# Performance work log

Hardware: AMD Instinct MI355X
Metric: run time of the kernel (lower is better)

The kernel has to match this reference:

```python
import jax, jax.numpy as jnp
import numpy as np
import math

EPS = 1e-5  # torch LayerNorm default


def entmax15(z):
    # Peters & Martins exact sort-based alpha=1.5 entmax along last axis.
    z = z / 2.0
    z = z - jnp.max(z, axis=-1, keepdims=True)
    zs = -jnp.sort(-z, axis=-1)                      # descending
    K = z.shape[-1]
    rho = jnp.arange(1, K + 1, dtype=z.dtype)
    mean = jnp.cumsum(zs, axis=-1) / rho
    mean_sq = jnp.cumsum(zs * zs, axis=-1) / rho
    ss = rho * (mean_sq - mean * mean)
    delta = jnp.clip((1.0 - ss) / rho, 0.0)
    tau = mean - jnp.sqrt(delta)
    k = jnp.sum(tau <= zs, axis=-1, keepdims=True)   # support size
    tau_star = jnp.take_along_axis(tau, k - 1, axis=-1)
    p = jnp.square(jnp.clip(z - tau_star, 0.0))
    return p


def mish(x):
    return x * jnp.tanh(jax.nn.softplus(x))


def layer_norm(x, g, b):
    mu = jnp.mean(x, axis=-1, keepdims=True)
    var = jnp.var(x, axis=-1, keepdims=True)
    return (x - mu) / jnp.sqrt(var + EPS) * g + b


def setup_inputs() -> dict:
    key = jax.random.key(0)
    D, H, F = 512, 8, 2048
    B, S = 8, 1024
    ks = jax.random.split(key, 16)
    s = 1.0 / math.sqrt(D)
    inp = {
        "x": jax.random.normal(ks[0], (B, S, D), jnp.float32),
        # weights stored [in, out]; y = x @ W + b
        "Wq": jax.random.normal(ks[1], (D, D), jnp.float32) * s,
        "bq": jnp.zeros((D,), jnp.float32),
        "Wk": jax.random.normal(ks[2], (D, D), jnp.float32) * s,
        "bk": jnp.zeros((D,), jnp.float32),
        "Wv": jax.random.normal(ks[3], (D, D), jnp.float32) * s,
        "bv": jnp.zeros((D,), jnp.float32),
        "Wo": jax.random.normal(ks[4], (D, D), jnp.float32) * s,
        "bo": jnp.zeros((D,), jnp.float32),
        "g1": jnp.ones((D,), jnp.float32),
        "be1": jnp.zeros((D,), jnp.float32),
        "W1": jax.random.normal(ks[5], (D, F), jnp.float32) * s,
        "b1": jnp.zeros((F,), jnp.float32),
        "W2": jax.random.normal(ks[6], (F, D), jnp.float32) * (1.0 / math.sqrt(F)),
        "b2": jnp.zeros((D,), jnp.float32),
        "g2": jnp.ones((D,), jnp.float32),
        "be2": jnp.zeros((D,), jnp.float32),
    }
    return inp


def reference(x, Wq, bq, Wk, bk, Wv, bv, Wo, bo, g1, be1, W1, b1, W2, b2, g2, be2):
    B, S, D = x.shape
    H = 8
    hd = D // H
    # multi-head self-attention (z = x)
    q = (x @ Wq + bq).reshape(B, S, H, hd).transpose(0, 2, 1, 3)
    k = (x @ Wk + bk).reshape(B, S, H, hd).transpose(0, 2, 1, 3)
    v = (x @ Wv + bv).reshape(B, S, H, hd).transpose(0, 2, 1, 3)
    scores = jnp.einsum("bhqd,bhkd->bhqk", q, k) / math.sqrt(hd)
    attn = entmax15(scores)
    out = jnp.einsum("bhqk,bhkd->bhqd", attn, v)
    out = out.transpose(0, 2, 1, 3).reshape(B, S, D)
    y = out @ Wo + bo
    x = x + layer_norm(y, g1, be1)
    # feed-forward with Mish
    y = mish(x @ W1 + b1) @ W2 + b2
    x = x + layer_norm(y, g2, be2)
    return x
```

## Files before the change

### kernel.cpp

```cpp
#include <hip/hip_runtime.h>


typedef float f32x4 __attribute__((ext_vector_type(4)));
typedef __bf16 b8 __attribute__((ext_vector_type(8)));

#define DEV static __device__ __forceinline__

DEV unsigned short f2bf(float f) {
  unsigned u = __float_as_uint(f);
  u += 0x7fffu + ((u >> 16) & 1u);
  return (unsigned short)(u >> 16);
}
DEV float bf2f(unsigned short b) { return __uint_as_float(((unsigned)b) << 16); }

DEV float mishf(float x) {
  if (x > 20.f) return x;
  float e = __expf(x);
  float u = 1.f + e;
  u *= u;
  return x * ((u - 1.f) / (u + 1.f));
}

DEV void async16(const void* g, void* l) {
  __builtin_amdgcn_global_load_lds(
      (const __attribute__((address_space(1))) unsigned int*)g,
      (__attribute__((address_space(3))) unsigned int*)l, 16, 0, 0);
}

template <int WM, int WN, int EPI, bool OUTBF>
__global__ __launch_bounds__(256) void gemm_bt(
    const unsigned short* __restrict__ A, const unsigned short* __restrict__ Bt,
    const float* __restrict__ bias, void* __restrict__ Cp,
    int K, int lda, int ldb, int ldc,
    long sA1, long sA2, long sB1, long sB2, long sC1, long sC2,
    int hdiv, float alpha) {
  constexpr int BM = WM * 64, BN = WN * 64;
  __shared__ unsigned short smA[BM * 32];
  __shared__ unsigned short smB[BN * 32];

  const int tid = threadIdx.x;
  const int lane = tid & 63;
  const int z = blockIdx.z;
  const long zi = z / hdiv, zr = z % hdiv;
  const unsigned short* Ab = A + zi * sA1 + zr * sA2 + (long)blockIdx.x * BM * lda;
  const unsigned short* Bb = Bt + zi * sB1 + zr * sB2 + (long)blockIdx.y * BN * ldb;

  int siA[WM];
  const unsigned short* gA[WM];
#pragma unroll
  for (int q = 0; q < WM; ++q) {
    int si = q * 256 + tid;
    int m = si >> 2, s = si & 3, g = s ^ ((m >> 1) & 3);
    siA[q] = si;
    gA[q] = Ab + (long)m * lda + g * 8;
  }
  int siB[WN];
  const unsigned short* gB[WN];
#pragma unroll
  for (int q = 0; q < WN; ++q) {
    int si = q * 256 + tid;
    int m = si >> 2, s = si & 3, g = s ^ ((m >> 1) & 3);
    siB[q] = si;
    gB[q] = Bb + (long)m * ldb + g * 8;
  }

  const int w = tid >> 6;
  const int wr = w / WN, wc = w % WN;
  const int fm = lane & 15, fg = lane >> 4;

  int aOff[4], bOff[4];
#pragma unroll
  for (int i = 0; i < 4; ++i) {
    int m = wr * 64 + i * 16 + fm;
    aOff[i] = (m * 4 + (fg ^ ((m >> 1) & 3))) * 8;
    int n = wc * 64 + i * 16 + fm;
    bOff[i] = (n * 4 + (fg ^ ((n >> 1) & 3))) * 8;
  }

  f32x4 acc[4][4];
#pragma unroll
  for (int i = 0; i < 4; ++i)
#pragma unroll
    for (int j = 0; j < 4; ++j) acc[i][j] = (f32x4){0.f, 0.f, 0.f, 0.f};

  for (int k0 = 0; k0 < K; k0 += 32) {
    __syncthreads();
#pragma unroll
    for (int q = 0; q < WM; ++q) async16(gA[q] + k0, (void*)&smA[siA[q] * 8]);
#pragma unroll
    for (int q = 0; q < WN; ++q) async16(gB[q] + k0, (void*)&smB[siB[q] * 8]);
    __syncthreads();

    b8 aF[4], bF[4];
#pragma unroll
    for (int i = 0; i < 4; ++i) aF[i] = *(const b8*)&smA[aOff[i]];
#pragma unroll
    for (int j = 0; j < 4; ++j) bF[j] = *(const b8*)&smB[bOff[j]];
#pragma unroll
    for (int i = 0; i < 4; ++i)
#pragma unroll
      for (int j = 0; j < 4; ++j)
        acc[i][j] = __builtin_amdgcn_mfma_f32_16x16x32_bf16(aF[i], bF[j], acc[i][j], 0, 0, 0);
  }

  const long cbase = zi * sC1 + zr * sC2;
  const int row0 = blockIdx.x * BM + wr * 64 + fg * 4;
  const int col0 = blockIdx.y * BN + wc * 64 + fm;
#pragma unroll
  for (int i = 0; i < 4; ++i) {
#pragma unroll
    for (int j = 0; j < 4; ++j) {
      const int col = col0 + j * 16;
      float bv = (EPI >= 1) ? bias[col] : 0.f;
#pragma unroll
      for (int r = 0; r < 4; ++r) {
        const int row = row0 + i * 16 + r;
        float v = acc[i][j][r] * alpha + bv;
        if (EPI == 2) v = mishf(v);
        const long idx = cbase + (long)row * ldc + col;
        if constexpr (OUTBF)
          ((unsigned short*)Cp)[idx] = f2bf(v);
        else
          ((float*)Cp)[idx] = v;
      }
    }
  }
}

__global__ __launch_bounds__(256) void entmax_rows(unsigned short* __restrict__ P) {
  const int tid = threadIdx.x, lane = tid & 63, wv = tid >> 6;
  const long row = (long)blockIdx.x * 4 + wv;
  unsigned short* p = P + row * 1024;

  union { uint4 v; unsigned short u[8]; } a, b;
  a.v = *(const uint4*)(p + lane * 16);
  b.v = *(const uint4*)(p + lane * 16 + 8);
  float zv[16];
#pragma unroll
  for (int i = 0; i < 8; ++i) {
    zv[i] = bf2f(a.u[i]);
    zv[8 + i] = bf2f(b.u[i]);
  }

  float m = zv[0];
#pragma unroll
  for (int i = 1; i < 16; ++i) m = fmaxf(m, zv[i]);
#pragma unroll
  for (int o = 32; o; o >>= 1) m = fmaxf(m, __shfl_xor(m, o));
#pragma unroll
  for (int i = 0; i < 16; ++i) zv[i] -= m;

  float tau = -1.f;
  int kprev = -1;
  for (int it = 0; it < 12; ++it) {
    float s1 = 0.f, s2 = 0.f;
    int k = 0;
#pragma unroll
    for (int i = 0; i < 16; ++i) {
      float h = zv[i] - tau;
      k += __popcll(__ballot(h > 0.f));
      float hp = fmaxf(h, 0.f);
      s1 += hp;
      s2 = fmaf(hp, hp, s2);
    }
#pragma unroll
    for (int o = 32; o; o >>= 1) {
      s1 += __shfl_xor(s1, o);
      s2 += __shfl_xor(s2, o);
    }
    if (k == kprev) break;
    kprev = k;
    float kf = (float)k;
    float disc = fmaxf(fmaf(s1, s1, -kf * (s2 - 1.f)), 0.f);
    tau += (s1 - __builtin_sqrtf(disc)) / kf;
  }

#pragma unroll
  for (int i = 0; i < 8; ++i) {
    float h0 = fmaxf(zv[i] - tau, 0.f);
    float h1 = fmaxf(zv[8 + i] - tau, 0.f);
    a.u[i] = f2bf(h0 * h0);
    b.u[i] = f2bf(h1 * h1);
  }
  *(uint4*)(p + lane * 16) = a.v;
  *(uint4*)(p + lane * 16 + 8) = b.v;
}

__global__ __launch_bounds__(256) void cast_f2b(const float* __restrict__ in,
                                                unsigned short* __restrict__ out, long n) {
  long i = ((long)blockIdx.x * 256 + threadIdx.x) * 4;
  if (i >= n) return;
  float4 v = *(const float4*)&in[i];
  unsigned lo = (unsigned)f2bf(v.x) | ((unsigned)f2bf(v.y) << 16);
  unsigned hi = (unsigned)f2bf(v.z) | ((unsigned)f2bf(v.w) << 16);
  uint2 p;
  p.x = lo;
  p.y = hi;
  *(uint2*)&out[i] = p;
}

__global__ __launch_bounds__(256) void concat3(const float* __restrict__ a,
                                               const float* __restrict__ b,
                                               const float* __restrict__ c,
                                               float* __restrict__ o) {
  int i = blockIdx.x * 256 + threadIdx.x;
  if (i < 512) o[i] = a[i];
  else if (i < 1024) o[i] = b[i - 512];
  else if (i < 1536) o[i] = c[i - 1024];
}

__global__ __launch_bounds__(256) void transpose_f2b(const float* __restrict__ in,
                                                     unsigned short* __restrict__ out,
                                                     int ldi, int ldo) {
  __shared__ float t[32][33];
  const int tx = threadIdx.x & 31, ty = threadIdx.x >> 5;
  const int r0 = blockIdx.y * 32, c0 = blockIdx.x * 32;
#pragma unroll
  for (int q = 0; q < 4; ++q) {
    int r = ty + q * 8;
    t[r][tx] = in[(long)(r0 + r) * ldi + c0 + tx];
  }
  __syncthreads();
#pragma unroll
  for (int q = 0; q < 4; ++q) {
    int r = ty + q * 8;
    out[(long)(c0 + r) * ldo + r0 + tx] = f2bf(t[tx][r]);
  }
}

__global__ __launch_bounds__(256) void transpose_b2b(const unsigned short* __restrict__ in,
                                                     unsigned short* __restrict__ out,
                                                     int ldi, int ldo, long i1, long i2,
                                                     long o1, long o2, int hdiv) {
  __shared__ unsigned short t[32][33];
  const int z = blockIdx.z;
  in += (long)(z / hdiv) * i1 + (long)(z % hdiv) * i2;
  out += (long)(z / hdiv) * o1 + (long)(z % hdiv) * o2;
  const int tx = threadIdx.x & 31, ty = threadIdx.x >> 5;
  const int r0 = blockIdx.y * 32, c0 = blockIdx.x * 32;
#pragma unroll
  for (int q = 0; q < 4; ++q) {
    int r = ty + q * 8;
    t[r][tx] = in[(long)(r0 + r) * ldi + c0 + tx];
  }
  __syncthreads();
#pragma unroll
  for (int q = 0; q < 4; ++q) {
    int r = ty + q * 8;
    out[(long)(c0 + r) * ldo + r0 + tx] = t[tx][r];
  }
}

template <bool WB, int NS>
__global__ __launch_bounds__(256) void ln_res(const float* __restrict__ xin,
                                              const float* __restrict__ y, long ystr,
                                              const float* __restrict__ ybias,
                                              const float* __restrict__ g,
                                              const float* __restrict__ be,
                                              float* __restrict__ xo,
                                              unsigned short* __restrict__ xob) {
  const int row = blockIdx.x, tid = threadIdx.x, lane = tid & 63, wv = tid >> 6;
  const long base = (long)row * 512 + tid * 2;
  const int c = tid * 2;
  float2 v = *(const float2*)&y[base];
#pragma unroll
  for (int j = 1; j < NS; ++j) {
    float2 u = *(const float2*)&y[base + j * ystr];
    v.x += u.x;
    v.y += u.y;
  }
  v.x += ybias[c];
  v.y += ybias[c + 1];
  float s1 = v.x + v.y, s2 = v.x * v.x + v.y * v.y;
  for (int o = 32; o; o >>= 1) {
    s1 += __shfl_xor(s1, o);
    s2 += __shfl_xor(s2, o);
  }
  __shared__ float red[4][2];
  if (lane == 0) {
    red[wv][0] = s1;
    red[wv][1] = s2;
  }
  __syncthreads();
  s1 = red[0][0] + red[1][0] + red[2][0] + red[3][0];
  s2 = red[0][1] + red[1][1] + red[2][1] + red[3][1];
  const float mu = s1 * (1.f / 512.f);
  const float rstd = rsqrtf(s2 * (1.f / 512.f) - mu * mu + 1e-5f);
  float2 xv = *(const float2*)&xin[base];
  float o0 = xv.x + (v.x - mu) * rstd * g[c] + be[c];
  float o1 = xv.y + (v.y - mu) * rstd * g[c + 1] + be[c + 1];
  float2 ov;
  ov.x = o0;
  ov.y = o1;
  *(float2*)&xo[base] = ov;
  if constexpr (WB) {
    unsigned pk = (unsigned)f2bf(o0) | ((unsigned)f2bf(o1) << 16);
    *(unsigned*)&xob[base] = pk;
  }
}

extern "C" void kernel_launch(void* const* d_in, const int* in_sizes, int n_in,
                              void* d_out, int out_size, void* d_ws, size_t ws_size,
                              hipStream_t stream) {
  const int B = 8, S = 1024, D = 512, H = 8, F = 2048;
  const int BS = B * S;
  const int N3 = 3 * D;

  const float* x = (const float*)d_in[0];
  const float* Wq = (const float*)d_in[1];
  const float* bq = (const float*)d_in[2];
  const float* Wk = (const float*)d_in[3];
  const float* bk = (const float*)d_in[4];
  const float* Wv = (const float*)d_in[5];
  const float* bv = (const float*)d_in[6];
  const float* Wo = (const float*)d_in[7];
  const float* bo = (const float*)d_in[8];
  const float* g1 = (const float*)d_in[9];
  const float* be1 = (const float*)d_in[10];
  const float* W1 = (const float*)d_in[11];
  const float* b1 = (const float*)d_in[12];
  const float* W2 = (const float*)d_in[13];
  const float* b2 = (const float*)d_in[14];
  const float* g2 = (const float*)d_in[15];
  const float* be2 = (const float*)d_in[16];
  float* out = (float*)d_out;

  char* w = (char*)d_ws;
  size_t off = 0;
  auto alloc = [&](size_t bytes) -> void* {
    void* p = w + off;
    off += bytes;
    off = (off + 255) & ~(size_t)255;
    return p;
  };

  unsigned short* xb = (unsigned short*)alloc((size_t)BS * D * 2);
  unsigned short* Wqkvt = (unsigned short*)alloc((size_t)N3 * D * 2);
  unsigned short* Wot = (unsigned short*)alloc((size_t)D * D * 2);
  unsigned short* W1t = (unsigned short*)alloc((size_t)F * D * 2);
  unsigned short* W2t = (unsigned short*)alloc((size_t)D * F * 2);
  float* bqkv = (float*)alloc((size_t)N3 * 4);
  unsigned short* QKVb = (unsigned short*)alloc((size_t)BS * N3 * 2);
  unsigned short* Vt = (unsigned short*)alloc((size_t)BS * D * 2);
  unsigned short* attn = (unsigned short*)alloc((size_t)BS * D * 2);
  unsigned short* P = (unsigned short*)alloc((size_t)B * H * S * S * 2);
  float* x1 = (float*)alloc((size_t)BS * D * 4);
  unsigned short* hb = (unsigned short*)alloc((size_t)BS * F * 2);
  unsigned short* x1b = xb;
  float* yp = (float*)P;
  const long PSTR = (long)BS * D;

  const long SS = (long)S * S;
  const long HSS = (long)H * SS;

  cast_f2b<<<(BS * D) / 1024, 256, 0, stream>>>(x, xb, (long)BS * D);
  transpose_f2b<<<dim3(16, 16, 1), 256, 0, stream>>>(Wq, Wqkvt, D, D);
  transpose_f2b<<<dim3(16, 16, 1), 256, 0, stream>>>(Wk, Wqkvt + (size_t)D * D, D, D);
  transpose_f2b<<<dim3(16, 16, 1), 256, 0, stream>>>(Wv, Wqkvt + (size_t)2 * D * D, D, D);
  transpose_f2b<<<dim3(16, 16, 1), 256, 0, stream>>>(Wo, Wot, D, D);
  transpose_f2b<<<dim3(F / 32, D / 32, 1), 256, 0, stream>>>(W1, W1t, F, D);
  transpose_f2b<<<dim3(D / 32, F / 32, 1), 256, 0, stream>>>(W2, W2t, D, F);
  concat3<<<6, 256, 0, stream>>>(bq, bk, bv, bqkv);

  gemm_bt<2, 2, 1, true><<<dim3(BS / 128, N3 / 128, 1), 256, 0, stream>>>(
      xb, Wqkvt, bqkv, QKVb, D, D, D, N3, 0, 0, 0, 0, 0, 0, 1, 1.f);

  transpose_b2b<<<dim3(2, 32, 64), 256, 0, stream>>>(
      QKVb + 1024, Vt, N3, S, (long)S * N3, 64, (long)8 * 64 * S, (long)64 * S, 8);

  gemm_bt<2, 2, 0, true><<<dim3(S / 128, S / 128, B * H), 256, 0, stream>>>(
      QKVb, QKVb + 512, nullptr, P, 64, N3, N3, S,
      (long)S * N3, 64, (long)S * N3, 64, HSS, SS, H, 1.f / 16.f);

  entmax_rows<<<(B * H * S) / 4, 256, 0, stream>>>(P);

  gemm_bt<4, 1, 0, true><<<dim3(S / 256, 1, B * H), 256, 0, stream>>>(
      P, Vt, nullptr, attn, S, S, S, D,
      HSS, SS, (long)8 * 64 * S, (long)64 * S, (long)S * D, 64, H, 1.f);

  gemm_bt<2, 2, 0, false><<<dim3(BS / 128, D / 128, 2), 256, 0, stream>>>(
      attn, Wot, nullptr, yp, D / 2, D, D, D, 0, D / 2, 0, D / 2, 0, PSTR, 2, 1.f);

  ln_res<true, 2><<<BS, 256, 0, stream>>>(x, yp, PSTR, bo, g1, be1, x1, x1b);

  gemm_bt<2, 2, 2, true><<<dim3(BS / 128, F / 128, 1), 256, 0, stream>>>(
      x1b, W1t, b1, hb, D, D, D, F, 0, 0, 0, 0, 0, 0, 1, 1.f);

  gemm_bt<2, 2, 0, false><<<dim3(BS / 128, D / 128, 4), 256, 0, stream>>>(
      hb, W2t, nullptr, yp, F / 4, F, F, D, 0, F / 4, 0, F / 4, 0, PSTR, 4, 1.f);

  ln_res<false, 4><<<BS, 256, 0, stream>>>(x1, yp, PSTR, b2, g2, be2, out, nullptr);
}
```

Before: 393.5 us.

## Merge prep kernels, pack entmax math into float2, halve W2 split-K

Fuses the cast, six weight transposes and bias concat into a single prep_all launch to cut launch overhead. The entmax row kernel now works on float2 pairs so the compiler can emit packed VALU ops, and it folds the max subtraction into the initial tau instead of shifting every element. The FFN down-projection split-K drops from 4 to 2, which halves the partial-sum traffic into LayerNorm but gives fewer blocks and longer K loops per block.

```diff
diff --git a/kernel.cpp b/kernel.cpp
--- a/kernel.cpp
+++ b/kernel.cpp
@@ -2,6 +2,7 @@
 
 
 typedef float f32x4 __attribute__((ext_vector_type(4)));
+typedef float f32x2 __attribute__((ext_vector_type(2)));
 typedef __bf16 b8 __attribute__((ext_vector_type(8)));
 
 #define DEV static __device__ __forceinline__
@@ -135,34 +136,37 @@
   union { uint4 v; unsigned short u[8]; } a, b;
   a.v = *(const uint4*)(p + lane * 16);
   b.v = *(const uint4*)(p + lane * 16 + 8);
-  float zv[16];
-#pragma unroll
-  for (int i = 0; i < 8; ++i) {
-    zv[i] = bf2f(a.u[i]);
-    zv[8 + i] = bf2f(b.u[i]);
-  }
-
-  float m = zv[0];
-#pragma unroll
-  for (int i = 1; i < 16; ++i) m = fmaxf(m, zv[i]);
+  f32x2 zp[8];
+#pragma unroll
+  for (int i = 0; i < 4; ++i) {
+    zp[i] = (f32x2){bf2f(a.u[2 * i]), bf2f(a.u[2 * i + 1])};
+    zp[4 + i] = (f32x2){bf2f(b.u[2 * i]), bf2f(b.u[2 * i + 1])};
+  }
+
+  f32x2 mv = zp[0];
+#pragma unroll
+  for (int i = 1; i < 8; ++i) mv = __builtin_elementwise_max(mv, zp[i]);
+  float m = fmaxf(mv.x, mv.y);
 #pragma unroll
   for (int o = 32; o; o >>= 1) m = fmaxf(m, __shfl_xor(m, o));
-#pragma unroll
-  for (int i = 0; i < 16; ++i) zv[i] -= m;
-
-  float tau = -1.f;
+
+  float tau = m - 1.f;
   int kprev = -1;
+  const f32x2 zero2 = (f32x2){0.f, 0.f};
   for (int it = 0; it < 12; ++it) {
-    float s1 = 0.f, s2 = 0.f;
+    const f32x2 t2 = (f32x2){tau, tau};
+    f32x2 s1v = zero2, s2v = zero2;
     int k = 0;
 #pragma unroll
-    for (int i = 0; i < 16; ++i) {
-      float h = zv[i] - tau;
-      k += __popcll(__ballot(h > 0.f));
-      float hp = fmaxf(h, 0.f);
-      s1 += hp;
-      s2 = fmaf(hp, hp, s2);
+    for (int i = 0; i < 8; ++i) {
+      f32x2 h = zp[i] - t2;
+      k += __popcll(__ballot(h.x > 0.f));
+      k += __popcll(__ballot(h.y > 0.f));
+      f32x2 hp = __builtin_elementwise_max(h, zero2);
+      s1v += hp;
+      s2v += hp * hp;
     }
+    float s1 = s1v.x + s1v.y, s2 = s2v.x + s2v.y;
 #pragma unroll
     for (int o = 32; o; o >>= 1) {
       s1 += __shfl_xor(s1, o);
@@ -175,46 +179,82 @@
     tau += (s1 - __builtin_sqrtf(disc)) / kf;
   }
 
-#pragma unroll
-  for (int i = 0; i < 8; ++i) {
-    float h0 = fmaxf(zv[i] - tau, 0.f);
-    float h1 = fmaxf(zv[8 + i] - tau, 0.f);
-    a.u[i] = f2bf(h0 * h0);
-    b.u[i] = f2bf(h1 * h1);
+  const f32x2 t2 = (f32x2){tau, tau};
+#pragma unroll
+  for (int i = 0; i < 4; ++i) {
+    f32x2 h0 = __builtin_elementwise_max(zp[i] - t2, zero2);
+    f32x2 h1 = __builtin_elementwise_max(zp[4 + i] - t2, zero2);
+    f32x2 p0 = h0 * h0, p1 = h1 * h1;
+    a.u[2 * i] = f2bf(p0.x);
+    a.u[2 * i + 1] = f2bf(p0.y);
+    b.u[2 * i] = f2bf(p1.x);
+    b.u[2 * i + 1] = f2bf(p1.y);
   }
   *(uint4*)(p + lane * 16) = a.v;
   *(uint4*)(p + lane * 16 + 8) = b.v;
 }
 
-__global__ __launch_bounds__(256) void cast_f2b(const float* __restrict__ in,
-                                                unsigned short* __restrict__ out, long n) {
-  long i = ((long)blockIdx.x * 256 + threadIdx.x) * 4;
-  if (i >= n) return;
-  float4 v = *(const float4*)&in[i];
-  unsigned lo = (unsigned)f2bf(v.x) | ((unsigned)f2bf(v.y) << 16);
-  unsigned hi = (unsigned)f2bf(v.z) | ((unsigned)f2bf(v.w) << 16);
-  uint2 p;
-  p.x = lo;
-  p.y = hi;
-  *(uint2*)&out[i] = p;
-}
-
-__global__ __launch_bounds__(256) void concat3(const float* __restrict__ a,
-                                               const float* __restrict__ b,
-                                               const float* __restrict__ c,
-                                               float* __restrict__ o) {
-  int i = blockIdx.x * 256 + threadIdx.x;
-  if (i < 512) o[i] = a[i];
-  else if (i < 1024) o[i] = b[i - 512];
-  else if (i < 1536) o[i] = c[i - 1024];
-}
-
-__global__ __launch_bounds__(256) void transpose_f2b(const float* __restrict__ in,
-                                                     unsigned short* __restrict__ out,
-                                                     int ldi, int ldo) {
+__global__ __launch_bounds__(256) void prep_all(
+    const float* __restrict__ x, unsigned short* __restrict__ xb,
+    const float* __restrict__ Wq, const float* __restrict__ Wk,
+    const float* __restrict__ Wv, const float* __restrict__ Wo,
+    const float* __restrict__ W1, const float* __restrict__ W2,
+    unsigned short* __restrict__ Wqkvt, unsigned short* __restrict__ Wot,
+    unsigned short* __restrict__ W1t, unsigned short* __restrict__ W2t,
+    const float* __restrict__ bq, const float* __restrict__ bk,
+    const float* __restrict__ bv, float* __restrict__ bqkv) {
   __shared__ float t[32][33];
-  const int tx = threadIdx.x & 31, ty = threadIdx.x >> 5;
-  const int r0 = blockIdx.y * 32, c0 = blockIdx.x * 32;
+  const int bid = blockIdx.x, tid = threadIdx.x;
+
+  if (bid < 4096) {
+    long i = ((long)bid * 256 + tid) * 4;
+    float4 v = *(const float4*)&x[i];
+    uint2 pk;
+    pk.x = (unsigned)f2bf(v.x) | ((unsigned)f2bf(v.y) << 16);
+    pk.y = (unsigned)f2bf(v.z) | ((unsigned)f2bf(v.w) << 16);
+    *(uint2*)&xb[i] = pk;
+    return;
+  }
+
+  const float* in;
+  unsigned short* out;
+  int ldi, ldo, bx, by;
+  if (bid < 5120) {
+    int t4 = (bid - 4096) >> 8, local = (bid - 4096) & 255;
+    const float* ins[4] = {Wq, Wk, Wv, Wo};
+    unsigned short* outs[4] = {Wqkvt, Wqkvt + 512 * 512, Wqkvt + 2 * 512 * 512, Wot};
+    in = ins[t4];
+    out = outs[t4];
+    ldi = 512;
+    ldo = 512;
+    bx = local & 15;
+    by = local >> 4;
+  } else if (bid < 6144) {
+    int local = bid - 5120;
+    in = W1;
+    out = W1t;
+    ldi = 2048;
+    ldo = 512;
+    bx = local & 63;
+    by = local >> 6;
+  } else if (bid < 7168) {
+    int local = bid - 6144;
+    in = W2;
+    out = W2t;
+    ldi = 512;
+    ldo = 2048;
+    bx = local & 15;
+    by = local >> 4;
+  } else {
+    int i = (bid - 7168) * 256 + tid;
+    if (i < 512) bqkv[i] = bq[i];
+    else if (i < 1024) bqkv[i] = bk[i - 512];
+    else if (i < 1536) bqkv[i] = bv[i - 1024];
+    return;
+  }
+
+  const int tx = tid & 31, ty = tid >> 5;
+  const int r0 = by * 32, c0 = bx * 32;
 #pragma unroll
   for (int q = 0; q < 4; ++q) {
     int r = ty + q * 8;
@@ -353,14 +393,8 @@
   const long SS = (long)S * S;
   const long HSS = (long)H * SS;
 
-  cast_f2b<<<(BS * D) / 1024, 256, 0, stream>>>(x, xb, (long)BS * D);
-  transpose_f2b<<<dim3(16, 16, 1), 256, 0, stream>>>(Wq, Wqkvt, D, D);
-  transpose_f2b<<<dim3(16, 16, 1), 256, 0, stream>>>(Wk, Wqkvt + (size_t)D * D, D, D);
-  transpose_f2b<<<dim3(16, 16, 1), 256, 0, stream>>>(Wv, Wqkvt + (size_t)2 * D * D, D, D);
-  transpose_f2b<<<dim3(16, 16, 1), 256, 0, stream>>>(Wo, Wot, D, D);
-  transpose_f2b<<<dim3(F / 32, D / 32, 1), 256, 0, stream>>>(W1, W1t, F, D);
-  transpose_f2b<<<dim3(D / 32, F / 32, 1), 256, 0, stream>>>(W2, W2t, D, F);
-  concat3<<<6, 256, 0, stream>>>(bq, bk, bv, bqkv);
+  prep_all<<<7174, 256, 0, stream>>>(x, xb, Wq, Wk, Wv, Wo, W1, W2,
+                                     Wqkvt, Wot, W1t, W2t, bq, bk, bv, bqkv);
 
   gemm_bt<2, 2, 1, true><<<dim3(BS / 128, N3 / 128, 1), 256, 0, stream>>>(
       xb, Wqkvt, bqkv, QKVb, D, D, D, N3, 0, 0, 0, 0, 0, 0, 1, 1.f);
@@ -386,8 +420,8 @@
   gemm_bt<2, 2, 2, true><<<dim3(BS / 128, F / 128, 1), 256, 0, stream>>>(
       x1b, W1t, b1, hb, D, D, D, F, 0, 0, 0, 0, 0, 0, 1, 1.f);
 
-  gemm_bt<2, 2, 0, false><<<dim3(BS / 128, D / 128, 4), 256, 0, stream>>>(
-      hb, W2t, nullptr, yp, F / 4, F, F, D, 0, F / 4, 0, F / 4, 0, PSTR, 4, 1.f);
-
-  ln_res<false, 4><<<BS, 256, 0, stream>>>(x1, yp, PSTR, b2, g2, be2, out, nullptr);
-}
+  gemm_bt<2, 2, 0, false><<<dim3(BS / 128, D / 128, 2), 256, 0, stream>>>(
+      hb, W2t, nullptr, yp, F / 2, F, F, D, 0, F / 2, 0, F / 2, 0, PSTR, 2, 1.f);
+
+  ln_res<false, 2><<<BS, 256, 0, stream>>>(x1, yp, PSTR, b2, g2, be2, out, nullptr);
+}
```

After: 376.2 us. -4.4%, faster.
